# Kernel optimization log

Measured on AMD Instinct MI355X. Metric: run time of the kernel, lower is better.

The kernel has to match this reference:

```python
import jax, jax.numpy as jnp
import numpy as np

S, L, E, H, HID, T = 4096, 16, 256, 512, 512, 50
CHAR_V = 128


def _lstm_scan(x, W_ih, W_hh, b):
    """x: [T, B, D] -> all hidden states [T, B, H]. PyTorch gate order i,f,g,o.
    b is the sum of torch's b_ih + b_hh (identical math)."""
    Hh = W_hh.shape[1]
    B = x.shape[1]

    def cell(carry, xt):
        h, c = carry
        g = xt @ W_ih.T + h @ W_hh.T + b  # [B, 4H]
        i, f, gg, o = jnp.split(g, 4, axis=-1)
        c = jax.nn.sigmoid(f) * c + jax.nn.sigmoid(i) * jnp.tanh(gg)
        h = jax.nn.sigmoid(o) * jnp.tanh(c)
        return (h, c), h

    init = (jnp.zeros((B, Hh), x.dtype), jnp.zeros((B, Hh), x.dtype))
    _, hs = jax.lax.scan(cell, init, x)
    return hs


def setup_inputs() -> dict:
    key = jax.random.key(0)
    ks = jax.random.split(key, 18)

    def p(k, shape):
        return jax.random.normal(k, shape, jnp.float32) * 0.05

    return {
        "chars": jax.random.randint(ks[0], (S, L), 0, CHAR_V),
        "char_lens": jax.random.randint(ks[1], (S,), 0, L),
        "char_table": p(ks[2], (CHAR_V, E)),
        "cW_ih": p(ks[3], (4 * E, E)),
        "cW_hh": p(ks[4], (4 * E, E)),
        "cb": p(ks[5], (4 * E,)),
        "W_ih0": p(ks[6], (2, 4 * H, E)),
        "W_hh0": p(ks[7], (2, 4 * H, H)),
        "b0": p(ks[8], (2, 4 * H)),
        "W_ih1": p(ks[9], (2, 4 * H, 2 * H)),
        "W_hh1": p(ks[10], (2, 4 * H, H)),
        "b1": p(ks[11], (2, 4 * H)),
        "fc1_w": p(ks[12], (HID, 2 * H)),
        "fc1_b": p(ks[13], (HID,)),
        "fc2_w": p(ks[14], (T, HID)),
        "fc2_b": p(ks[15], (T,)),
    }


def reference(chars, char_lens, char_table, cW_ih, cW_hh, cb,
              W_ih0, W_hh0, b0, W_ih1, W_hh1, b1,
              fc1_w, fc1_b, fc2_w, fc2_b):
    n_words = chars.shape[0]
    # --- char LSTM: batched over all words (replaces per-word python loop) ---
    emb = char_table[chars]                               # [S, L, E]
    hs = _lstm_scan(emb.transpose(1, 0, 2), cW_ih, cW_hh, cb)  # [L, S, E]
    lens = jnp.maximum(char_lens, 1)                      # every word has >=1 char
    word_emb = hs[lens - 1, jnp.arange(n_words)]          # hn per word: [S, E]

    # --- 2-layer bidirectional sentence LSTM, batch = 1 ---
    x = word_emb[:, None, :]                              # [S, 1, E]

    def bi_layer(x, Wih, Whh, b):
        fwd = _lstm_scan(x, Wih[0], Whh[0], b[0])
        bwd = _lstm_scan(x[::-1], Wih[1], Whh[1], b[1])[::-1]
        return jnp.concatenate([fwd, bwd], axis=-1)       # [S, 1, 2H]

    x = bi_layer(x, W_ih0, W_hh0, b0)
    x = bi_layer(x, W_ih1, W_hh1, b1)

    # --- MLP head ---
    out = x[:, 0, :]                                      # [S, 2H]
    out = jnp.tanh(out @ fc1_w.T + fc1_b)                 # [S, HID]
    return out @ fc2_w.T + fc2_b                          # [S, T]
```

## Files before the change

### kernel.cpp

```cpp
#include <hip/hip_runtime.h>
#include <math.h>
#include <stdint.h>


#define NPOS 4096
#define GDIM 2048

typedef short short8 __attribute__((ext_vector_type(8)));
typedef float f32x4 __attribute__((ext_vector_type(4)));

__device__ __forceinline__ float sigf(float x) { return 1.0f / (1.0f + __expf(-x)); }
__device__ __forceinline__ float tanh_fast(float x) {
  float e = __expf(2.f * x);
  return 1.f - 2.f / (e + 1.f);
}
__device__ __forceinline__ unsigned int pack_bf16(float a, float b) {
  unsigned int ua = __float_as_uint(a), ub = __float_as_uint(b);
  ua = (ua + 0x7fffu + ((ua >> 16) & 1u)) >> 16;
  ub = (ub + 0x7fffu + ((ub >> 16) & 1u)) >> 16;
  return ua | (ub << 16);
}

__global__ __launch_bounds__(256) void build_wt_kernel(
    const float* __restrict__ cWih, const float* __restrict__ cWhh,
    float* __restrict__ Wt)
{
  __shared__ float tile[64][65];
  const int k0 = blockIdx.x * 64;
  const int g0 = blockIdx.y * 64;
  const float* src = (k0 < 256) ? cWih : cWhh;
  const int sk0 = k0 & 255;
  for (int i = threadIdx.x; i < 64 * 64; i += 256) {
    int r = i >> 6, cc = i & 63;
    tile[r][cc] = src[(size_t)(g0 + r) * 256 + sk0 + cc];
  }
  __syncthreads();
  for (int i = threadIdx.x; i < 64 * 64; i += 256) {
    int kk = i >> 6, gg = i & 63;
    Wt[(size_t)(k0 + kk) * 1024 + g0 + gg] = tile[gg][kk];
  }
}

__global__ __launch_bounds__(256) void char_lstm_kernel(
    const int* __restrict__ chars, const int* __restrict__ lens,
    const float* __restrict__ table, const float* __restrict__ Wt,
    const float* __restrict__ cb, float* __restrict__ word_emb)
{
  __shared__ float u[8][512];
  __shared__ float wt[8][1024];
  __shared__ int sidx[8];
  const int tid = threadIdx.x;
  const int ch = tid;
  const int w0 = blockIdx.x * 8;
  if (tid < 8) { int l = lens[w0 + tid]; sidx[tid] = (l < 1 ? 1 : l) - 1; }
  float c[8], acc0[8], acc1[8], acc2[8], acc3[8];
  #pragma unroll
  for (int w = 0; w < 8; ++w) { u[w][256 + ch] = 0.f; c[w] = 0.f; }
  const float cb0 = cb[ch], cb1 = cb[256 + ch], cb2 = cb[512 + ch], cb3 = cb[768 + ch];

  for (int t = 0; t < 16; ++t) {
    for (int w = 0; w < 8; ++w) {
      int cid = chars[(w0 + w) * 16 + t];
      u[w][ch] = table[(size_t)cid * 256 + ch];
    }
    #pragma unroll
    for (int w = 0; w < 8; ++w) { acc0[w] = cb0; acc1[w] = cb1; acc2[w] = cb2; acc3[w] = cb3; }
    for (int k0 = 0; k0 < 512; k0 += 8) {
      #pragma unroll
      for (int r = 0; r < 8; ++r)
        ((float4*)&wt[r][0])[tid] = ((const float4*)(Wt + (size_t)(k0 + r) * 1024))[tid];
      __syncthreads();
      #pragma unroll
      for (int kk = 0; kk < 8; ++kk) {
        const float wv0 = wt[kk][ch], wv1 = wt[kk][256 + ch];
        const float wv2 = wt[kk][512 + ch], wv3 = wt[kk][768 + ch];
        #pragma unroll
        for (int w = 0; w < 8; ++w) {
          const float uv = u[w][k0 + kk];
          acc0[w] = fmaf(wv0, uv, acc0[w]);
          acc1[w] = fmaf(wv1, uv, acc1[w]);
          acc2[w] = fmaf(wv2, uv, acc2[w]);
          acc3[w] = fmaf(wv3, uv, acc3[w]);
        }
      }
      __syncthreads();
    }
    #pragma unroll
    for (int w = 0; w < 8; ++w) {
      float iv = sigf(acc0[w]), fv = sigf(acc1[w]);
      float gv = tanhf(acc2[w]), ov = sigf(acc3[w]);
      c[w] = fv * c[w] + iv * gv;
      float h = ov * tanhf(c[w]);
      u[w][256 + ch] = h;
      if (t == sidx[w]) word_emb[(size_t)(w0 + w) * 256 + ch] = h;
    }
  }
}

#define SW(c) ((c) + (((c) >> 3) << 2))
template <int SPLIT, int ACT, int PERM>
__global__ __launch_bounds__(256) void gemm_kernel(
    const float* __restrict__ A, const float* __restrict__ A2,
    const float* __restrict__ B, const float* __restrict__ bias,
    float* __restrict__ C, int M, int N, int K)
{
  __shared__ float At[8 * 192];
  __shared__ float Bt[8 * 192];
  const int tid = threadIdx.x;
  const int bm0 = blockIdx.x * 128, bn0 = blockIdx.y * 128;
  float acc[8][8];
  #pragma unroll
  for (int i = 0; i < 8; ++i)
    #pragma unroll
    for (int j = 0; j < 8; ++j) acc[i][j] = 0.f;
  const int sr = tid >> 1;
  const int sk = (tid & 1) * 4;
  const int tm = (tid >> 4) * 8, tn = (tid & 15) * 8;
  const int swsr = SW(sr);
  const int stm = SW(tm), stn = SW(tn);
  for (int k0 = 0; k0 < K; k0 += 8) {
    const int kg = k0 + sk;
    float4 av;
    if (SPLIT) {
      const float* srcp = (kg < 512) ? A : A2;
      av = *(const float4*)(srcp + (size_t)(bm0 + sr) * 512 + (kg & 511));
    } else {
      av = *(const float4*)(A + (size_t)(bm0 + sr) * K + kg);
    }
    float4 bv = {0.f, 0.f, 0.f, 0.f};
    if (bn0 + sr < N) bv = *(const float4*)(B + (size_t)(bn0 + sr) * K + kg);
    At[(sk + 0) * 192 + swsr] = av.x; At[(sk + 1) * 192 + swsr] = av.y;
    At[(sk + 2) * 192 + swsr] = av.z; At[(sk + 3) * 192 + swsr] = av.w;
    Bt[(sk + 0) * 192 + swsr] = bv.x; Bt[(sk + 1) * 192 + swsr] = bv.y;
    Bt[(sk + 2) * 192 + swsr] = bv.z; Bt[(sk + 3) * 192 + swsr] = bv.w;
    __syncthreads();
    #pragma unroll
    for (int kk = 0; kk < 8; ++kk) {
      float a[8], b[8];
      *(float4*)&a[0] = *(const float4*)&At[kk * 192 + stm];
      *(float4*)&a[4] = *(const float4*)&At[kk * 192 + stm + 4];
      *(float4*)&b[0] = *(const float4*)&Bt[kk * 192 + stn];
      *(float4*)&b[4] = *(const float4*)&Bt[kk * 192 + stn + 4];
      #pragma unroll
      for (int i = 0; i < 8; ++i)
        #pragma unroll
        for (int j = 0; j < 8; ++j) acc[i][j] = fmaf(a[i], b[j], acc[i][j]);
    }
    __syncthreads();
  }
  #pragma unroll
  for (int i = 0; i < 8; ++i) {
    const int m = bm0 + tm + i;
    float* crow = C + (size_t)m * N;
    #pragma unroll
    for (int j = 0; j < 8; ++j) {
      const int n = bn0 + tn + j;
      if (n < N) {
        float v = acc[i][j] + bias[n];
        if (ACT) v = tanhf(v);
        if (PERM) crow[((n & 511) << 2) | (n >> 9)] = v;
        else      crow[n] = v;
      }
    }
  }
}

template <int SPLIT, int ACT, int PERM>
__global__ __launch_bounds__(256) void mfgemm_kernel(
    const float* __restrict__ A, const float* __restrict__ A2,
    const float* __restrict__ B, const float* __restrict__ bias,
    float* __restrict__ C, int M, int N, int K)
{
  __shared__ unsigned short AL[128 * 40];
  __shared__ unsigned short BL[128 * 40];
  const int tid = threadIdx.x;
  const int bm0 = blockIdx.x * 128, bn0 = blockIdx.y * 128;
  const int srow = tid >> 1;
  const int sk = (tid & 1) * 16;
  const int lane = tid & 63;
  const int wid = tid >> 6;
  const int wm0 = (wid >> 1) * 64;
  const int wn0 = (wid & 1) * 64;
  const int lrow = lane & 15;
  const int lk = (lane >> 4) * 8;

  f32x4 acc[4][4];
  #pragma unroll
  for (int i = 0; i < 4; ++i)
    #pragma unroll
    for (int j = 0; j < 4; ++j) acc[i][j] = (f32x4){0.f, 0.f, 0.f, 0.f};

  for (int k0 = 0; k0 < K; k0 += 32) {
    const int kg = k0 + sk;
    float av[16], bv[16];
    if (SPLIT) {
      const float* srcp = (kg < 512) ? A : A2;
      const float* ap = srcp + (size_t)(bm0 + srow) * 512 + (kg & 511);
      #pragma unroll
      for (int i = 0; i < 4; ++i) *(float4*)&av[4 * i] = ((const float4*)ap)[i];
      const float* srcq = (kg < 512) ? B : (B + 512);
      (void)srcq;
    } else {
      const float* ap = A + (size_t)(bm0 + srow) * K + kg;
      #pragma unroll
      for (int i = 0; i < 4; ++i) *(float4*)&av[4 * i] = ((const float4*)ap)[i];
    }
    {
      const float* bp = B + (size_t)(bn0 + srow) * K + kg;
      #pragma unroll
      for (int i = 0; i < 4; ++i) *(float4*)&bv[4 * i] = ((const float4*)bp)[i];
    }
    unsigned int pa[8], pb[8];
    #pragma unroll
    for (int i = 0; i < 8; ++i) {
      pa[i] = pack_bf16(av[2 * i], av[2 * i + 1]);
      pb[i] = pack_bf16(bv[2 * i], bv[2 * i + 1]);
    }
    unsigned short* adst = &AL[srow * 40 + sk];
    unsigned short* bdst = &BL[srow * 40 + sk];
    *(uint4*)adst       = *(uint4*)&pa[0];
    *(uint4*)(adst + 8) = *(uint4*)&pa[4];
    *(uint4*)bdst       = *(uint4*)&pb[0];
    *(uint4*)(bdst + 8) = *(uint4*)&pb[4];
    __syncthreads();

    short8 af[4], bf[4];
    #pragma unroll
    for (int mi = 0; mi < 4; ++mi)
      af[mi] = *(const short8*)&AL[(wm0 + mi * 16 + lrow) * 40 + lk];
    #pragma unroll
    for (int ni = 0; ni < 4; ++ni)
      bf[ni] = *(const short8*)&BL[(wn0 + ni * 16 + lrow) * 40 + lk];
    #pragma unroll
    for (int mi = 0; mi < 4; ++mi)
      #pragma unroll
      for (int ni = 0; ni < 4; ++ni)
        acc[mi][ni] = __builtin_amdgcn_mfma_f32_16x16x32_bf16(
            af[mi], bf[ni], acc[mi][ni], 0, 0, 0);
    __syncthreads();
  }

  #pragma unroll
  for (int mi = 0; mi < 4; ++mi) {
    #pragma unroll
    for (int ni = 0; ni < 4; ++ni) {
      const int n = bn0 + wn0 + ni * 16 + (lane & 15);
      const float bz = bias[n];
      const int nw = PERM ? (((n & 511) << 2) | (n >> 9)) : n;
      #pragma unroll
      for (int r = 0; r < 4; ++r) {
        const int m = bm0 + wm0 + mi * 16 + (lane >> 4) * 4 + r;
        float v = acc[mi][ni][r] + bz;
        if (ACT) v = tanhf(v);
        C[(size_t)m * N + nw] = v;
      }
    }
  }
}

__global__ __launch_bounds__(512) void scan_kernel(
    const float* __restrict__ Xf, const float* __restrict__ Xb,
    const float* __restrict__ Whf, const float* __restrict__ Whb,
    unsigned long long* __restrict__ Tf, unsigned long long* __restrict__ Tb,
    float* __restrict__ Hf, float* __restrict__ Hb)
{
  __shared__ float lds_h[2][576];
  const int tid = threadIdx.x;
  const int dir = blockIdx.x & 1;
  const int wg  = blockIdx.x >> 1;
  const float* X = dir ? Xb : Xf;
  const float* Wh = dir ? Whb : Whf;
  unsigned long long* T = dir ? Tb : Tf;
  float* Hd = dir ? Hb : Hf;

  const int row8 = tid >> 3;
  const int klane = tid & 7;
  const int u = row8 >> 2, g = row8 & 3;
  const int R = g * 512 + wg * 16 + u;

  float wreg[64];
  {
    const float* wrow = Wh + (size_t)R * 512 + klane * 64;
    #pragma unroll
    for (int i = 0; i < 16; ++i) {
      float4 v = ((const float4*)wrow)[i];
      wreg[4 * i] = v.x; wreg[4 * i + 1] = v.y; wreg[4 * i + 2] = v.z; wreg[4 * i + 3] = v.w;
    }
  }
  const int l0 = 72 * klane;
  const int l1 = l0 + 36;
  const int la = tid + ((tid >> 5) << 2);
  const int rep = wg & 3;

  for (int i = tid; i < 576; i += 512) lds_h[0][i] = 0.f;

  const bool xl = (klane == 0);
  const int xoff = wg * 64 + row8;
  float xcur = 0.f, xnxt = 0.f;
  if (xl) {
    xcur = X[(size_t)(dir ? NPOS - 1 : 0) * GDIM + xoff];
    xnxt = X[(size_t)(dir ? NPOS - 2 : 1) * GDIM + xoff];
  }
  float creg = 0.f;
  __syncthreads();

  for (int s = 0; s < NPOS; ++s) {
    const int p = dir ? (NPOS - 1 - s) : s;
    if (s > 0) {
      const unsigned int tg = (unsigned int)s;
      const unsigned long long* w =
          T + (size_t)((rep << 1) | ((s - 1) & 1)) * 512 + tid;
      unsigned long long v;
      do { v = __hip_atomic_load(w, __ATOMIC_RELAXED, __HIP_MEMORY_SCOPE_AGENT); }
      while ((unsigned int)(v >> 32) != tg);
      lds_h[s & 1][la] = __uint_as_float((unsigned int)v);
    }
    __syncthreads();
    const float* hb = &lds_h[s & 1][0];
    float sA = xl ? xcur : 0.f, sB = 0.f, sC = 0.f, sD = 0.f;
    if (xl) {
      xcur = xnxt;
      if (s + 2 < NPOS) xnxt = X[(size_t)(dir ? NPOS - 3 - s : s + 2) * GDIM + xoff];
    }
    #pragma unroll
    for (int i = 0; i < 4; ++i) {
      float4 a = *(const float4*)&hb[l0 + 4 * i];
      sA = fmaf(wreg[4 * i + 0], a.x, sA);
      sA = fmaf(wreg[4 * i + 1], a.y, sA);
      sA = fmaf(wreg[4 * i + 2], a.z, sA);
      sA = fmaf(wreg[4 * i + 3], a.w, sA);
      float4 b = *(const float4*)&hb[l0 + 16 + 4 * i];
      sB = fmaf(wreg[16 + 4 * i + 0], b.x, sB);
      sB = fmaf(wreg[16 + 4 * i + 1], b.y, sB);
      sB = fmaf(wreg[16 + 4 * i + 2], b.z, sB);
      sB = fmaf(wreg[16 + 4 * i + 3], b.w, sB);
      float4 c = *(const float4*)&hb[l1 + 4 * i];
      sC = fmaf(wreg[32 + 4 * i + 0], c.x, sC);
      sC = fmaf(wreg[32 + 4 * i + 1], c.y, sC);
      sC = fmaf(wreg[32 + 4 * i + 2], c.z, sC);
      sC = fmaf(wreg[32 + 4 * i + 3], c.w, sC);
      float4 d = *(const float4*)&hb[l1 + 16 + 4 * i];
      sD = fmaf(wreg[48 + 4 * i + 0], d.x, sD);
      sD = fmaf(wreg[48 + 4 * i + 1], d.y, sD);
      sD = fmaf(wreg[48 + 4 * i + 2], d.z, sD);
      sD = fmaf(wreg[48 + 4 * i + 3], d.w, sD);
    }
    float sum = (sA + sB) + (sC + sD);
    sum += __shfl_xor(sum, 1);
    sum += __shfl_xor(sum, 2);
    sum += __shfl_xor(sum, 4);
    const int base = (tid & 63) & ~31;
    float gf = __shfl(sum, base + 8);
    float gg = __shfl(sum, base + 16);
    float go = __shfl(sum, base + 24);
    if ((tid & 31) == 0) {
      float iv = sigf(sum), fv = sigf(gf), gv = tanh_fast(gg), ov = sigf(go);
      creg = fv * creg + iv * gv;
      float h = ov * tanh_fast(creg);
      const int j = wg * 16 + u;
      unsigned long long pack = ((unsigned long long)(unsigned int)(s + 1) << 32)
                              | (unsigned long long)__float_as_uint(h);
      #pragma unroll
      for (int r2 = 0; r2 < 4; ++r2)
        __hip_atomic_store(&T[(size_t)((r2 << 1) | (s & 1)) * 512 + j], pack,
                           __ATOMIC_RELAXED, __HIP_MEMORY_SCOPE_AGENT);
      Hd[(size_t)p * 512 + j] = h;
    }
  }
}

extern "C" void kernel_launch(void* const* d_in, const int* in_sizes, int n_in,
                              void* d_out, int out_size, void* d_ws, size_t ws_size,
                              hipStream_t stream) {
  const int* chars = (const int*)d_in[0];
  const int* lens = (const int*)d_in[1];
  const float* table = (const float*)d_in[2];
  const float* cWih = (const float*)d_in[3];
  const float* cWhh = (const float*)d_in[4];
  const float* cb = (const float*)d_in[5];
  const float* Wih0 = (const float*)d_in[6];
  const float* Whh0 = (const float*)d_in[7];
  const float* b0 = (const float*)d_in[8];
  const float* Wih1 = (const float*)d_in[9];
  const float* Whh1 = (const float*)d_in[10];
  const float* b1 = (const float*)d_in[11];
  const float* fc1w = (const float*)d_in[12];
  const float* fc1b = (const float*)d_in[13];
  const float* fc2w = (const float*)d_in[14];
  const float* fc2b = (const float*)d_in[15];
  float* out = (float*)d_out;

  char* ws = (char*)d_ws;
  size_t off = 0;
  auto alloc = [&](size_t bytes) -> void* {
    void* p = ws + off;
    off += (bytes + 255) & ~(size_t)255;
    return p;
  };
  float* word_emb = (float*)alloc((size_t)4096 * 256 * 4);
  float* X0f = (float*)alloc((size_t)4096 * 2048 * 4);
  float* X0b = (float*)alloc((size_t)4096 * 2048 * 4);
  float* H0f = (float*)alloc((size_t)4096 * 512 * 4);
  float* H0b = (float*)alloc((size_t)4096 * 512 * 4);
  float* H1f = (float*)alloc((size_t)4096 * 512 * 4);
  float* H1b = (float*)alloc((size_t)4096 * 512 * 4);
  float* fc1out = (float*)alloc((size_t)4096 * 512 * 4);
  float* Wt = (float*)alloc((size_t)512 * 1024 * 4);
  unsigned long long* Tall = (unsigned long long*)alloc((size_t)4 * 4096 * 8);
  unsigned long long* T0f = Tall;
  unsigned long long* T0b = Tall + 4096;
  unsigned long long* T1f = Tall + 8192;
  unsigned long long* T1b = Tall + 12288;
  if (off > ws_size) return;

  hipMemsetAsync(Tall, 0, (size_t)4 * 4096 * 8, stream);

  build_wt_kernel<<<dim3(8, 16), 256, 0, stream>>>(cWih, cWhh, Wt);
  char_lstm_kernel<<<512, 256, 0, stream>>>(chars, lens, table, Wt, cb, word_emb);

  mfgemm_kernel<0, 0, 1><<<dim3(32, 16), 256, 0, stream>>>(
      word_emb, nullptr, Wih0, b0, X0f, 4096, 2048, 256);
  mfgemm_kernel<0, 0, 1><<<dim3(32, 16), 256, 0, stream>>>(
      word_emb, nullptr, Wih0 + (size_t)2048 * 256, b0 + 2048, X0b, 4096, 2048, 256);
  scan_kernel<<<64, 512, 0, stream>>>(X0f, X0b, Whh0, Whh0 + (size_t)2048 * 512,
                                      T0f, T0b, H0f, H0b);

  mfgemm_kernel<1, 0, 1><<<dim3(32, 16), 256, 0, stream>>>(
      H0f, H0b, Wih1, b1, X0f, 4096, 2048, 1024);
  mfgemm_kernel<1, 0, 1><<<dim3(32, 16), 256, 0, stream>>>(
      H0f, H0b, Wih1 + (size_t)2048 * 1024, b1 + 2048, X0b, 4096, 2048, 1024);
  scan_kernel<<<64, 512, 0, stream>>>(X0f, X0b, Whh1, Whh1 + (size_t)2048 * 512,
                                      T1f, T1b, H1f, H1b);

  mfgemm_kernel<1, 1, 0><<<dim3(32, 4), 256, 0, stream>>>(
      H1f, H1b, fc1w, fc1b, fc1out, 4096, 512, 1024);
  gemm_kernel<0, 0, 0><<<dim3(32, 1), 256, 0, stream>>>(
      fc1out, nullptr, fc2w, fc2b, out, 4096, 50, 512);
}
```

Before: 15.44 ms.

## Rewrite char LSTM as bf16 MFMA kernel over 32 words per block

Replaces the FP32 scalar-FMA char LSTM (8 words per block, weights staged through shared memory) with an MFMA bf16 kernel that processes 32 words per block, reading packed bf16 [gate x k] weights straight from global/L2. Gate pre-activations are written to shared memory as bf16 and the cell update uses fast exp-based tanh. This aims to cut the compute-bound char-LSTM stage. In exchange it loses precision (bf16 inputs, hidden state and gate values) and launches only 128 blocks, which may underfill the GPU.

```diff
diff --git a/kernel.cpp b/kernel.cpp
--- a/kernel.cpp
+++ b/kernel.cpp
@@ -20,80 +20,103 @@
   ub = (ub + 0x7fffu + ((ub >> 16) & 1u)) >> 16;
   return ua | (ub << 16);
 }
-
-__global__ __launch_bounds__(256) void build_wt_kernel(
+__device__ __forceinline__ unsigned short bf16_1(float a) {
+  unsigned int ua = __float_as_uint(a);
+  return (unsigned short)((ua + 0x7fffu + ((ua >> 16) & 1u)) >> 16);
+}
+__device__ __forceinline__ float bf2f(unsigned short s) {
+  return __uint_as_float(((unsigned int)s) << 16);
+}
+
+__global__ __launch_bounds__(256) void build_wc_kernel(
     const float* __restrict__ cWih, const float* __restrict__ cWhh,
-    float* __restrict__ Wt)
+    unsigned int* __restrict__ Wc)
 {
-  __shared__ float tile[64][65];
-  const int k0 = blockIdx.x * 64;
-  const int g0 = blockIdx.y * 64;
-  const float* src = (k0 < 256) ? cWih : cWhh;
-  const int sk0 = k0 & 255;
-  for (int i = threadIdx.x; i < 64 * 64; i += 256) {
-    int r = i >> 6, cc = i & 63;
-    tile[r][cc] = src[(size_t)(g0 + r) * 256 + sk0 + cc];
-  }
-  __syncthreads();
-  for (int i = threadIdx.x; i < 64 * 64; i += 256) {
-    int kk = i >> 6, gg = i & 63;
-    Wt[(size_t)(k0 + kk) * 1024 + g0 + gg] = tile[gg][kk];
-  }
-}
-
-__global__ __launch_bounds__(256) void char_lstm_kernel(
+  const int idx = blockIdx.x * 256 + threadIdx.x;
+  const int g = idx >> 8;
+  const int k = (idx & 255) * 2;
+  const float* src = (k < 256) ? (cWih + (size_t)g * 256 + k)
+                               : (cWhh + (size_t)g * 256 + (k - 256));
+  Wc[idx] = pack_bf16(src[0], src[1]);
+}
+
+__global__ __launch_bounds__(256) void mfchar_kernel(
     const int* __restrict__ chars, const int* __restrict__ lens,
-    const float* __restrict__ table, const float* __restrict__ Wt,
+    const float* __restrict__ table, const unsigned short* __restrict__ Wc,
     const float* __restrict__ cb, float* __restrict__ word_emb)
 {
-  __shared__ float u[8][512];
-  __shared__ float wt[8][1024];
-  __shared__ int sidx[8];
+  __shared__ unsigned short uL[32][520];
+  __shared__ unsigned short gL[32][1032];
+  __shared__ int sidx[32];
   const int tid = threadIdx.x;
-  const int ch = tid;
-  const int w0 = blockIdx.x * 8;
-  if (tid < 8) { int l = lens[w0 + tid]; sidx[tid] = (l < 1 ? 1 : l) - 1; }
-  float c[8], acc0[8], acc1[8], acc2[8], acc3[8];
-  #pragma unroll
-  for (int w = 0; w < 8; ++w) { u[w][256 + ch] = 0.f; c[w] = 0.f; }
-  const float cb0 = cb[ch], cb1 = cb[256 + ch], cb2 = cb[512 + ch], cb3 = cb[768 + ch];
+  const int lane = tid & 63;
+  const int wv = tid >> 6;
+  const int w0 = blockIdx.x * 32;
+  if (tid < 32) { int l = lens[w0 + tid]; sidx[tid] = (l < 1 ? 1 : l) - 1; }
+  for (int i = tid; i < 32 * 256; i += 256) uL[i >> 8][256 + (i & 255)] = 0;
+
+  float bz[16];
+  #pragma unroll
+  for (int ni = 0; ni < 16; ++ni) bz[ni] = cb[wv * 256 + ni * 16 + (lane & 15)];
+
+  float c[32];
+  #pragma unroll
+  for (int w = 0; w < 32; ++w) c[w] = 0.f;
+
+  const int arow = lane & 15;
+  const int akk = (lane >> 4) * 8;
 
   for (int t = 0; t < 16; ++t) {
-    for (int w = 0; w < 8; ++w) {
-      int cid = chars[(w0 + w) * 16 + t];
-      u[w][ch] = table[(size_t)cid * 256 + ch];
-    }
-    #pragma unroll
-    for (int w = 0; w < 8; ++w) { acc0[w] = cb0; acc1[w] = cb1; acc2[w] = cb2; acc3[w] = cb3; }
-    for (int k0 = 0; k0 < 512; k0 += 8) {
-      #pragma unroll
-      for (int r = 0; r < 8; ++r)
-        ((float4*)&wt[r][0])[tid] = ((const float4*)(Wt + (size_t)(k0 + r) * 1024))[tid];
-      __syncthreads();
-      #pragma unroll
-      for (int kk = 0; kk < 8; ++kk) {
-        const float wv0 = wt[kk][ch], wv1 = wt[kk][256 + ch];
-        const float wv2 = wt[kk][512 + ch], wv3 = wt[kk][768 + ch];
+    for (int w = 0; w < 32; ++w) {
+      const int cid = chars[(w0 + w) * 16 + t];
+      uL[w][tid] = bf16_1(table[(size_t)cid * 256 + tid]);
+    }
+    __syncthreads();
+
+    f32x4 acc[2][16];
+    #pragma unroll
+    for (int mi = 0; mi < 2; ++mi)
+      #pragma unroll
+      for (int ni = 0; ni < 16; ++ni)
+        acc[mi][ni] = (f32x4){bz[ni], bz[ni], bz[ni], bz[ni]};
+    for (int kt = 0; kt < 16; ++kt) {
+      short8 af0 = *(const short8*)&uL[arow][kt * 32 + akk];
+      short8 af1 = *(const short8*)&uL[16 + arow][kt * 32 + akk];
+      #pragma unroll
+      for (int ni = 0; ni < 16; ++ni) {
+        const unsigned short* bp =
+            Wc + (size_t)(wv * 256 + ni * 16 + arow) * 512 + kt * 32 + akk;
+        short8 bf = *(const short8*)bp;
+        acc[0][ni] = __builtin_amdgcn_mfma_f32_16x16x32_bf16(af0, bf, acc[0][ni], 0, 0, 0);
+        acc[1][ni] = __builtin_amdgcn_mfma_f32_16x16x32_bf16(af1, bf, acc[1][ni], 0, 0, 0);
+      }
+    }
+    #pragma unroll
+    for (int mi = 0; mi < 2; ++mi)
+      #pragma unroll
+      for (int ni = 0; ni < 16; ++ni) {
+        const int col = wv * 256 + ni * 16 + (lane & 15);
         #pragma unroll
-        for (int w = 0; w < 8; ++w) {
-          const float uv = u[w][k0 + kk];
-          acc0[w] = fmaf(wv0, uv, acc0[w]);
-          acc1[w] = fmaf(wv1, uv, acc1[w]);
-          acc2[w] = fmaf(wv2, uv, acc2[w]);
-          acc3[w] = fmaf(wv3, uv, acc3[w]);
+        for (int r = 0; r < 4; ++r) {
+          const int row = mi * 16 + (lane >> 4) * 4 + r;
+          gL[row][col] = bf16_1(acc[mi][ni][r]);
         }
       }
-      __syncthreads();
-    }
-    #pragma unroll
-    for (int w = 0; w < 8; ++w) {
-      float iv = sigf(acc0[w]), fv = sigf(acc1[w]);
-      float gv = tanhf(acc2[w]), ov = sigf(acc3[w]);
+    __syncthreads();
+
+    const int j = tid;
+    #pragma unroll 4
+    for (int w = 0; w < 32; ++w) {
+      const float iv = sigf(bf2f(gL[w][j]));
+      const float fv = sigf(bf2f(gL[w][256 + j]));
+      const float gv = tanh_fast(bf2f(gL[w][512 + j]));
+      const float ov = sigf(bf2f(gL[w][768 + j]));
       c[w] = fv * c[w] + iv * gv;
-      float h = ov * tanhf(c[w]);
-      u[w][256 + ch] = h;
-      if (t == sidx[w]) word_emb[(size_t)(w0 + w) * 256 + ch] = h;
-    }
+      const float h = ov * tanh_fast(c[w]);
+      uL[w][256 + j] = bf16_1(h);
+      if (t == sidx[w]) word_emb[(size_t)(w0 + w) * 256 + j] = h;
+    }
+    __syncthreads();
   }
 }
 
@@ -198,8 +221,6 @@
       const float* ap = srcp + (size_t)(bm0 + srow) * 512 + (kg & 511);
       #pragma unroll
       for (int i = 0; i < 4; ++i) *(float4*)&av[4 * i] = ((const float4*)ap)[i];
-      const float* srcq = (kg < 512) ? B : (B + 512);
-      (void)srcq;
     } else {
       const float* ap = A + (size_t)(bm0 + srow) * K + kg;
       #pragma unroll
@@ -405,7 +426,7 @@
   float* H1f = (float*)alloc((size_t)4096 * 512 * 4);
   float* H1b = (float*)alloc((size_t)4096 * 512 * 4);
   float* fc1out = (float*)alloc((size_t)4096 * 512 * 4);
-  float* Wt = (float*)alloc((size_t)512 * 1024 * 4);
+  unsigned int* Wc = (unsigned int*)alloc((size_t)1024 * 512 * 2);
   unsigned long long* Tall = (unsigned long long*)alloc((size_t)4 * 4096 * 8);
   unsigned long long* T0f = Tall;
   unsigned long long* T0b = Tall + 4096;
@@ -415,8 +436,9 @@
 
   hipMemsetAsync(Tall, 0, (size_t)4 * 4096 * 8, stream);
 
-  build_wt_kernel<<<dim3(8, 16), 256, 0, stream>>>(cWih, cWhh, Wt);
-  char_lstm_kernel<<<512, 256, 0, stream>>>(chars, lens, table, Wt, cb, word_emb);
+  build_wc_kernel<<<1024, 256, 0, stream>>>(cWih, cWhh, Wc);
+  mfchar_kernel<<<128, 256, 0, stream>>>(chars, lens, table,
+                                         (const unsigned short*)Wc, cb, word_emb);
 
   mfgemm_kernel<0, 0, 1><<<dim3(32, 16), 256, 0, stream>>>(
       word_emb, nullptr, Wih0, b0, X0f, 4096, 2048, 256);
```

New measurement: 13.94 ms. 9.7% less time.
